# Kernel tuning notes

Hardware: AMD Instinct MI355X
Metric: run time of the kernel (lower is better)

## Reference

```python
import jax, jax.numpy as jnp
import numpy as np

B, S, E, H = 2, 1024, 1024, 16
Dh = E // H


def setup_inputs() -> dict:
    key = jax.random.key(0)
    ks = jax.random.split(key, 32)
    sc = 1.0 / np.sqrt(E)  # xavier-ish scale
    inp = {}
    names_x = ["x_q_a", "x_q_b", "x_kv_a", "x_kv_b"]
    for i, n in enumerate(names_x):
        inp[n] = jax.random.normal(ks[i], (B, S, E), jnp.float32)
    # causal mask, broadcastable to (B, H, S, S); masked where == 0
    inp["mask"] = jnp.tril(jnp.ones((S, S), jnp.int32))[None, None, :, :]
    inp["layer_theta"] = jnp.float32(0.3)
    inp["thetas_head"] = 0.1 * jax.random.normal(ks[4], (H,), jnp.float32)
    i = 5
    for p in ["q", "k", "v", "o"]:
        inp[p + "_wa"] = sc * jax.random.normal(ks[i], (E, E), jnp.float32); i += 1
        inp[p + "_wb"] = sc * jax.random.normal(ks[i], (E, E), jnp.float32); i += 1
        inp[p + "_ba"] = jnp.zeros((E,), jnp.float32)
        inp[p + "_bb"] = jnp.zeros((E,), jnp.float32)
    return inp


def _qc_dense(xa, xb, wa, wb, ba, bb, j2):
    # F.linear: x @ W.T + b ; j2 is a scalar so (Wb*j2) factors out
    out_a = xa @ wa.T + ba + (xb @ wb.T) * j2
    out_b = xa @ wb.T + bb + xb @ wa.T
    return out_a, out_b


def _shape(x):
    # (B,S,E) -> (B,H,S,Dh)
    return x.reshape(B, S, H, Dh).transpose(0, 2, 1, 3)


def _unshape(x):
    return x.transpose(0, 2, 1, 3).reshape(B, S, E)


def _rope(x):
    # standard rotate-half RoPE on last dim, positions over axis -2
    inv_freq = 1.0 / (10000.0 ** (jnp.arange(0, Dh, 2, dtype=jnp.float32) / Dh))
    ang = jnp.arange(S, dtype=jnp.float32)[:, None] * inv_freq[None, :]  # (S, Dh/2)
    cos = jnp.concatenate([jnp.cos(ang), jnp.cos(ang)], axis=-1)  # (S, Dh)
    sin = jnp.concatenate([jnp.sin(ang), jnp.sin(ang)], axis=-1)
    x1, x2 = x[..., : Dh // 2], x[..., Dh // 2:]
    rot = jnp.concatenate([-x2, x1], axis=-1)
    return x * cos + rot * sin


def reference(x_q_a, x_q_b, x_kv_a, x_kv_b, mask, layer_theta, thetas_head,
              q_wa, q_wb, q_ba, q_bb, k_wa, k_wb, k_ba, k_bb,
              v_wa, v_wb, v_ba, v_bb, o_wa, o_wb, o_ba, o_bb):
    j2 = jnp.sin(2.0 * layer_theta) - 1.0
    qa, qb = _qc_dense(x_q_a, x_q_b, q_wa, q_wb, q_ba, q_bb, j2)
    ka, kb = _qc_dense(x_kv_a, x_kv_b, k_wa, k_wb, k_ba, k_bb, j2)
    va, vb = _qc_dense(x_kv_a, x_kv_b, v_wa, v_wb, v_ba, v_bb, j2)
    qa, qb = _rope(_shape(qa)), _rope(_shape(qb))
    ka, kb = _rope(_shape(ka)), _rope(_shape(kb))
    va, vb = _shape(va), _shape(vb)
    j2h = (jnp.sin(2.0 * thetas_head) - 1.0).reshape(1, H, 1, 1)
    # dual QC score matrices (B,H,S,S)
    s_a = jnp.einsum("bhqd,bhkd->bhqk", qa, ka) + jnp.einsum("bhqd,bhkd->bhqk", qb, kb) * j2h
    s_b = jnp.einsum("bhqd,bhkd->bhqk", qa, kb) + jnp.einsum("bhqd,bhkd->bhqk", qb, ka)
    mag = jnp.sqrt(s_a * s_a + s_b * s_b + 1e-8) / np.sqrt(Dh)
    mag = jnp.where(mask == 0, -1e9, mag)
    attn = jax.nn.softmax(mag, axis=-1)
    out_a = _unshape(jnp.einsum("bhqk,bhkd->bhqd", attn, va))
    out_b = _unshape(jnp.einsum("bhqk,bhkd->bhqd", attn, vb))
    return _qc_dense(out_a, out_b, o_wa, o_wb, o_ba, o_bb, j2)
```

## Files before the change

kernel.cpp:

```cpp
#include <hip/hip_runtime.h>
#include <math.h>
#include <stdint.h>

#define BATCH 2
#define SEQ   1024
#define EMB   1024
#define NH    16
#define DH    64
#define BSE   (BATCH*SEQ*EMB)
#define MROWS (BATCH*SEQ)

typedef unsigned short u16;
typedef __attribute__((ext_vector_type(8))) short short8;
typedef __attribute__((ext_vector_type(4))) float f32x4;

__device__ __forceinline__ float bf2f(u16 u) {
    return __uint_as_float(((unsigned int)u) << 16);
}
__device__ __forceinline__ u16 f2bf(float f) {
    unsigned int x = __float_as_uint(f);
    x += 0x7FFFu + ((x >> 16) & 1u);
    return (u16)(x >> 16);
}

__device__ __forceinline__ void async_copy16(const void* g, void* l) {
    __builtin_amdgcn_global_load_lds(
        (const __attribute__((address_space(1))) unsigned int*)g,
        (__attribute__((address_space(3))) unsigned int*)l,
        16, 0, 0);
}

struct PackArgs {
    const float* src[20];
    u16*         dst[20];
    int          scaled[20];
};

__global__ __launch_bounds__(256) void pack_kernel(PackArgs pa, const float* __restrict__ theta)
{
    const int e = blockIdx.y;
    const size_t i = ((size_t)blockIdx.x * 256 + threadIdx.x) * 4;
    float sc = 1.0f;
    if (pa.scaled[e]) sc = sinf(2.0f * theta[0]) - 1.0f;
    float4 v = *(const float4*)(pa.src[e] + i);
    ushort4 o;
    o.x = f2bf(v.x * sc); o.y = f2bf(v.y * sc);
    o.z = f2bf(v.z * sc); o.w = f2bf(v.w * sc);
    *(ushort4*)(pa.dst[e] + i) = o;
}

struct GemmArgs {
    const u16*   A1s[8];
    const u16*   A2s[8];
    const u16*   Blo[8];
    const u16*   Bhi[8];
    const float* bias[8];
    void*        dst[8];
    int          mode[8];
};

template<int SPLITK>
__global__ __launch_bounds__(256) void mfma_gemm(GemmArgs ga)
{
    __shared__ u16 sA[128][32];
    __shared__ u16 sB[128][32];

    const int t    = threadIdx.x;
    const int lane = t & 63;
    const int w    = t >> 6;
    const int wx   = w & 1;
    const int wy   = w >> 1;
    const int n0   = blockIdx.y * 128;
    const int m0   = blockIdx.x * 128;
    const int ko   = (SPLITK == 2) ? blockIdx.z : 0;
    const int seg  = n0 >> 10;
    const int nloc = n0 & 1023;

    const int srow = t >> 2;
    const int sb   = (t & 3) * 16;

    f32x4 acc[4][4] = {};

    const char* A1 = (const char*)ga.A1s[seg];
    const char* A2 = (const char*)ga.A2s[seg];
    const char* Bl = (const char*)ga.Blo[seg];
    const char* Bh = (const char*)ga.Bhi[seg];
    if (SPLITK == 2 && ko) { A1 = A2; Bl = Bh; }

    const int frow = lane & 15;
    const int quad = lane >> 4;

    const int NKT = (SPLITK == 2) ? 32 : 64;
    for (int kt = 0; kt < NKT; ++kt) {
        const char* As = (SPLITK == 1 && (kt & 32)) ? A2 : A1;
        const char* Bs = (SPLITK == 1 && (kt & 32)) ? Bh : Bl;
        const size_t kbyte = (size_t)(kt & 31) * 64;

        __syncthreads();
        #pragma unroll
        for (int r = 0; r < 2; ++r) {
            const int row = r*64 + srow;
            const int ldsoff = (r*64 + w*16) * 64;
            async_copy16(As + (size_t)(m0 + row)*2048 + kbyte + sb,
                         (char*)&sA[0][0] + ldsoff);
            async_copy16(Bs + (size_t)(nloc + row)*2048 + kbyte + sb,
                         (char*)&sB[0][0] + ldsoff);
        }
        __syncthreads();

        short8 af[4], bfr[4];
        #pragma unroll
        for (int i = 0; i < 4; ++i)
            af[i] = *(const short8*)&sA[wy*64 + i*16 + frow][quad*8];
        #pragma unroll
        for (int j = 0; j < 4; ++j)
            bfr[j] = *(const short8*)&sB[wx*64 + j*16 + frow][quad*8];

        #pragma unroll
        for (int i = 0; i < 4; ++i)
            #pragma unroll
            for (int j = 0; j < 4; ++j)
                acc[i][j] = __builtin_amdgcn_mfma_f32_16x16x32_bf16(
                                af[i], bfr[j], acc[i][j], 0, 0, 0);
    }

    const float* bias = ga.bias[seg];
    const int mode = ga.mode[seg];

    #pragma unroll
    for (int j = 0; j < 4; ++j) {
        const int c = nloc + wx*64 + j*16 + frow;
        const float bv = (SPLITK == 2 && ko) ? 0.0f : bias[c];
        #pragma unroll
        for (int i = 0; i < 4; ++i) {
            #pragma unroll
            for (int reg = 0; reg < 4; ++reg) {
                const int m = m0 + wy*64 + i*16 + quad*4 + reg;
                const float val = acc[i][j][reg] + bv;
                if (mode == 1) {
                    if (SPLITK == 2)
                        atomicAdd((float*)ga.dst[seg] + (size_t)m*1024 + c, val);
                    else
                        ((float*)ga.dst[seg])[(size_t)m*1024 + c] = val;
                } else if (mode == 2) {
                    ((u16*)ga.dst[seg])[((size_t)(m >> 10) << 20) + (size_t)c*1024 + (m & 1023)] = f2bf(val);
                } else {
                    ((u16*)ga.dst[seg])[(size_t)m*1024 + c] = f2bf(val);
                }
            }
        }
    }
}

__global__ __launch_bounds__(256) void rope_kernel(
    u16* qa, u16* qb, u16* ka, u16* kb)
{
    u16* p;
    switch (blockIdx.y) {
        case 0:  p = qa; break;
        case 1:  p = qb; break;
        case 2:  p = ka; break;
        default: p = kb; break;
    }
    const int i   = blockIdx.x * 256 + threadIdx.x;
    const int d   = i & 31;
    const int hh  = (i >> 5) & (NH - 1);
    const int row = i >> 9;
    const int s   = row & (SEQ - 1);
    const size_t base = (size_t)row * EMB + hh * DH;

    float x1 = bf2f(p[base + d]);
    float x2 = bf2f(p[base + d + 32]);
    const float invf_rev = expf(-(float)d * 0.28782313662425576f) * 0.15915494309189535f;
    float rev = (float)s * invf_rev;
    rev -= floorf(rev);
    const float sn = __builtin_amdgcn_sinf(rev);
    const float cs = __builtin_amdgcn_cosf(rev);
    p[base + d]      = f2bf(x1 * cs - x2 * sn);
    p[base + d + 32] = f2bf(x2 * cs + x1 * sn);
}

__global__ __launch_bounds__(256) void attn_mfma(
    const u16* __restrict__ qa, const u16* __restrict__ qb,
    const u16* __restrict__ ka, const u16* __restrict__ kb,
    const u16* __restrict__ vat, const u16* __restrict__ vbt,
    const float* __restrict__ thetas,
    u16* __restrict__ oa, u16* __restrict__ ob)
{
    __shared__ u16 sKa[64][64];
    __shared__ u16 sKb[64][64];
    __shared__ u16 sVa[64][64];
    __shared__ u16 sVb[64][64];
    __shared__ u16 sP[4][16][72];

    const int t    = threadIdx.x;
    const int lane = t & 63;
    const int w    = t >> 6;
    const int L15  = lane & 15;
    const int quad = lane >> 4;

    const int bid  = blockIdx.x;
    const int aa   = (bid >> 5) & 7;
    const int qt   = (bid >> 8) ? aa : (15 - aa);
    const int bh   = bid & 31;
    const int h    = bh & 15;
    const int b    = bh >> 4;

    const float j2h = sinf(2.0f * thetas[h]) - 1.0f;

    const int   qrow  = qt*64 + w*16 + L15;
    const size_t qbase = (size_t)(b*SEQ + qrow) * EMB + h*DH;
    short8 fqa[2], fqb[2], fjqb[2];
    fqa[0] = *(const short8*)(qa + qbase + quad*8);
    fqa[1] = *(const short8*)(qa + qbase + 32 + quad*8);
    fqb[0] = *(const short8*)(qb + qbase + quad*8);
    fqb[1] = *(const short8*)(qb + qbase + 32 + quad*8);
    #pragma unroll
    for (int s2 = 0; s2 < 2; ++s2) {
        short8 src = fqb[s2], dst;
        #pragma unroll
        for (int j = 0; j < 8; ++j)
            dst[j] = (short)f2bf(bf2f((u16)src[j]) * j2h);
        fjqb[s2] = dst;
    }

    f32x4 acc_a[4] = {};
    f32x4 acc_b[4] = {};
    float l_lane[4] = {0.f, 0.f, 0.f, 0.f};

    const int subrow = lane >> 3;
    const int g      = (lane & 7) ^ subrow;
    const int swz    = L15 & 7;

    for (int kt = 0; kt <= qt; ++kt) {
        __syncthreads();
        #pragma unroll
        for (int i = 0; i < 2; ++i) {
            const int row = w*16 + i*8 + subrow;
            const int ldsoff = (w*16 + i*8) * 128;
            const size_t ktok = (size_t)(b*SEQ + kt*64 + row);
            async_copy16((const char*)ka + ktok*2048 + h*128 + g*16,
                         (char*)&sKa[0][0] + ldsoff);
            async_copy16((const char*)kb + ktok*2048 + h*128 + g*16,
                         (char*)&sKb[0][0] + ldsoff);
            const size_t vrow = (size_t)b*1048576 + (size_t)(h*64 + row)*1024 + kt*64;
            async_copy16((const char*)vat + vrow*2 + g*16,
                         (char*)&sVa[0][0] + ldsoff);
            async_copy16((const char*)vbt + vrow*2 + g*16,
                         (char*)&sVb[0][0] + ldsoff);
        }
        __syncthreads();

        f32x4 sa[4] = {}, sb[4] = {};
        #pragma unroll
        for (int n = 0; n < 4; ++n) {
            const u16* rKa = &sKa[n*16 + L15][0];
            const u16* rKb = &sKb[n*16 + L15][0];
            short8 ka0 = *(const short8*)(rKa + (( quad      ^ swz) << 3));
            short8 ka1 = *(const short8*)(rKa + (((4 + quad) ^ swz) << 3));
            short8 kb0 = *(const short8*)(rKb + (( quad      ^ swz) << 3));
            short8 kb1 = *(const short8*)(rKb + (((4 + quad) ^ swz) << 3));
            sa[n] = __builtin_amdgcn_mfma_f32_16x16x32_bf16(fqa[0],  ka0, sa[n], 0, 0, 0);
            sa[n] = __builtin_amdgcn_mfma_f32_16x16x32_bf16(fqa[1],  ka1, sa[n], 0, 0, 0);
            sa[n] = __builtin_amdgcn_mfma_f32_16x16x32_bf16(fjqb[0], kb0, sa[n], 0, 0, 0);
            sa[n] = __builtin_amdgcn_mfma_f32_16x16x32_bf16(fjqb[1], kb1, sa[n], 0, 0, 0);
            sb[n] = __builtin_amdgcn_mfma_f32_16x16x32_bf16(fqa[0],  kb0, sb[n], 0, 0, 0);
            sb[n] = __builtin_amdgcn_mfma_f32_16x16x32_bf16(fqa[1],  kb1, sb[n], 0, 0, 0);
            sb[n] = __builtin_amdgcn_mfma_f32_16x16x32_bf16(fqb[0],  ka0, sb[n], 0, 0, 0);
            sb[n] = __builtin_amdgcn_mfma_f32_16x16x32_bf16(fqb[1],  ka1, sb[n], 0, 0, 0);
        }

        float p[4][4];
        if (kt == qt) {
            #pragma unroll
            for (int n = 0; n < 4; ++n)
                #pragma unroll
                for (int r = 0; r < 4; ++r) {
                    const float A = sa[n][r], B = sb[n][r];
                    const float mag = __builtin_amdgcn_sqrtf(A*A + B*B + 1e-8f) * 0.125f;
                    const bool masked = (n*16 + L15) > (w*16 + quad*4 + r);
                    p[n][r] = masked ? 0.0f
                                     : __builtin_amdgcn_exp2f(mag * 1.44269504f);
                }
        } else {
            #pragma unroll
            for (int n = 0; n < 4; ++n)
                #pragma unroll
                for (int r = 0; r < 4; ++r) {
                    const float A = sa[n][r], B = sb[n][r];
                    const float mag = __builtin_amdgcn_sqrtf(A*A + B*B + 1e-8f) * 0.125f;
                    p[n][r] = __builtin_amdgcn_exp2f(mag * 1.44269504f);
                }
        }
        #pragma unroll
        for (int r = 0; r < 4; ++r)
            l_lane[r] += (p[0][r] + p[1][r]) + (p[2][r] + p[3][r]);

        #pragma unroll
        for (int n = 0; n < 4; ++n)
            #pragma unroll
            for (int r = 0; r < 4; ++r)
                sP[w][quad*4 + r][n*16 + L15] = f2bf(p[n][r]);

        short8 pf0 = *(const short8*)&sP[w][L15][quad*8];
        short8 pf1 = *(const short8*)&sP[w][L15][32 + quad*8];

        #pragma unroll
        for (int n = 0; n < 4; ++n) {
            const u16* rVa = &sVa[n*16 + L15][0];
            const u16* rVb = &sVb[n*16 + L15][0];
            short8 va0 = *(const short8*)(rVa + (( quad      ^ swz) << 3));
            short8 va1 = *(const short8*)(rVa + (((4 + quad) ^ swz) << 3));
            short8 vb0 = *(const short8*)(rVb + (( quad      ^ swz) << 3));
            short8 vb1 = *(const short8*)(rVb + (((4 + quad) ^ swz) << 3));
            acc_a[n] = __builtin_amdgcn_mfma_f32_16x16x32_bf16(pf0, va0, acc_a[n], 0, 0, 0);
            acc_a[n] = __builtin_amdgcn_mfma_f32_16x16x32_bf16(pf1, va1, acc_a[n], 0, 0, 0);
            acc_b[n] = __builtin_amdgcn_mfma_f32_16x16x32_bf16(pf0, vb0, acc_b[n], 0, 0, 0);
            acc_b[n] = __builtin_amdgcn_mfma_f32_16x16x32_bf16(pf1, vb1, acc_b[n], 0, 0, 0);
        }
    }

    float inv[4];
    #pragma unroll
    for (int r = 0; r < 4; ++r) {
        float l = l_lane[r];
        #pragma unroll
        for (int off = 8; off >= 1; off >>= 1)
            l += __shfl_xor(l, off, 64);
        inv[r] = 1.0f / l;
    }

    #pragma unroll
    for (int reg = 0; reg < 4; ++reg) {
        const size_t tok = (size_t)(b*SEQ + qt*64 + w*16 + quad*4 + reg);
        #pragma unroll
        for (int n = 0; n < 4; ++n) {
            const size_t idx = tok*EMB + h*DH + n*16 + L15;
            oa[idx] = f2bf(acc_a[n][reg] * inv[reg]);
            ob[idx] = f2bf(acc_b[n][reg] * inv[reg]);
        }
    }
}

extern "C" void kernel_launch(void* const* d_in, const int* in_sizes, int n_in,
                              void* d_out, int out_size, void* d_ws, size_t ws_size,
                              hipStream_t stream)
{
    const float* x_q_a  = (const float*)d_in[0];
    const float* x_q_b  = (const float*)d_in[1];
    const float* x_kv_a = (const float*)d_in[2];
    const float* x_kv_b = (const float*)d_in[3];
    const float* theta    = (const float*)d_in[5];
    const float* thetas_h = (const float*)d_in[6];
    const float* q_wa = (const float*)d_in[7];
    const float* q_wb = (const float*)d_in[8];
    const float* q_ba = (const float*)d_in[9];
    const float* q_bb = (const float*)d_in[10];
    const float* k_wa = (const float*)d_in[11];
    const float* k_wb = (const float*)d_in[12];
    const float* k_ba = (const float*)d_in[13];
    const float* k_bb = (const float*)d_in[14];
    const float* v_wa = (const float*)d_in[15];
    const float* v_wb = (const float*)d_in[16];
    const float* v_ba = (const float*)d_in[17];
    const float* v_bb = (const float*)d_in[18];
    const float* o_wa = (const float*)d_in[19];
    const float* o_wb = (const float*)d_in[20];
    const float* o_ba = (const float*)d_in[21];
    const float* o_bb = (const float*)d_in[22];

    u16* W = (u16*)d_ws;
    const size_t XN = (size_t)BSE;
    const size_t WN = (size_t)EMB*EMB;
    u16* xq_a16  = W;
    u16* xq_b16  = W + XN;
    u16* xkv_a16 = W + 2*XN;
    u16* xkv_b16 = W + 3*XN;
    u16* wbase   = W + 4*XN;
    u16* q_wa16  = wbase;
    u16* q_wb16  = wbase + WN;
    u16* k_wa16  = wbase + 2*WN;
    u16* k_wb16  = wbase + 3*WN;
    u16* v_wa16  = wbase + 4*WN;
    u16* v_wb16  = wbase + 5*WN;
    u16* o_wa16  = wbase + 6*WN;
    u16* o_wb16  = wbase + 7*WN;
    u16* q_wbs16 = wbase + 8*WN;
    u16* k_wbs16 = wbase + 9*WN;
    u16* v_wbs16 = wbase + 10*WN;
    u16* o_wbs16 = wbase + 11*WN;
    u16* qkv     = wbase + 12*WN;
    u16* qa16 = qkv;
    u16* qb16 = qkv + XN;
    u16* ka16 = qkv + 2*XN;
    u16* kb16 = qkv + 3*XN;
    u16* vat16 = qkv + 4*XN;
    u16* vbt16 = qkv + 5*XN;
    u16* ao16 = xq_a16;
    u16* bo16 = xq_b16;

    float* out_a = (float*)d_out;
    float* out_b = out_a + (size_t)BSE;

    PackArgs pa;
    int si = 0;
    auto add = [&](const float* s, u16* d, int scaled, int chunks) {
        for (int c = 0; c < chunks; ++c) {
            pa.src[si] = s + (size_t)c * WN;
            pa.dst[si] = d + (size_t)c * WN;
            pa.scaled[si] = scaled;
            ++si;
        }
    };
    add(x_q_a,  xq_a16,  0, 2);
    add(x_q_b,  xq_b16,  0, 2);
    add(x_kv_a, xkv_a16, 0, 2);
    add(x_kv_b, xkv_b16, 0, 2);
    add(q_wa, q_wa16, 0, 1);  add(q_wb, q_wb16, 0, 1);
    add(k_wa, k_wa16, 0, 1);  add(k_wb, k_wb16, 0, 1);
    add(v_wa, v_wa16, 0, 1);  add(v_wb, v_wb16, 0, 1);
    add(o_wa, o_wa16, 0, 1);  add(o_wb, o_wb16, 0, 1);
    add(q_wb, q_wbs16, 1, 1); add(k_wb, k_wbs16, 1, 1);
    add(v_wb, v_wbs16, 1, 1); add(o_wb, o_wbs16, 1, 1);
    pack_kernel<<<dim3(WN/1024, 20), 256, 0, stream>>>(pa, theta);

    hipMemsetAsync(d_out, 0, (size_t)out_size * sizeof(float), stream);

    GemmArgs g12;
    const u16* a1s[6] = { xq_a16, xq_a16, xkv_a16, xkv_a16, xkv_a16, xkv_a16 };
    const u16* a2s[6] = { xq_b16, xq_b16, xkv_b16, xkv_b16, xkv_b16, xkv_b16 };
    const u16* blo[6] = { q_wa16, q_wb16, k_wa16, k_wb16, v_wa16, v_wb16 };
    const u16* bhi[6] = { q_wbs16, q_wa16, k_wbs16, k_wa16, v_wbs16, v_wa16 };
    const float* bia[6] = { q_ba, q_bb, k_ba, k_bb, v_ba, v_bb };
    void* dsts[6] = { qa16, qb16, ka16, kb16, vat16, vbt16 };
    const int modes[6] = { 0, 0, 0, 0, 2, 2 };
    for (int s = 0; s < 6; ++s) {
        g12.A1s[s] = a1s[s]; g12.A2s[s] = a2s[s];
        g12.Blo[s] = blo[s]; g12.Bhi[s] = bhi[s];
        g12.bias[s] = bia[s]; g12.dst[s] = dsts[s]; g12.mode[s] = modes[s];
    }
    for (int s = 6; s < 8; ++s) {
        g12.A1s[s] = a1s[0]; g12.A2s[s] = a2s[0];
        g12.Blo[s] = blo[0]; g12.Bhi[s] = bhi[0];
        g12.bias[s] = bia[0]; g12.dst[s] = dsts[0]; g12.mode[s] = 0;
    }
    mfma_gemm<1><<<dim3(MROWS/128, 48), 256, 0, stream>>>(g12);

    rope_kernel<<<dim3((BATCH*SEQ*NH*32)/256, 4), 256, 0, stream>>>(qa16, qb16, ka16, kb16);

    attn_mfma<<<BATCH*NH*(SEQ/64), 256, 0, stream>>>(qa16, qb16, ka16, kb16,
                                                     vat16, vbt16, thetas_h, ao16, bo16);

    GemmArgs g3;
    for (int s = 0; s < 8; ++s) {
        g3.A1s[s] = ao16; g3.A2s[s] = bo16;
        g3.Blo[s] = o_wa16; g3.Bhi[s] = o_wbs16;
        g3.bias[s] = o_ba; g3.dst[s] = out_a; g3.mode[s] = 1;
    }
    g3.Blo[1] = o_wb16; g3.Bhi[1] = o_wa16; g3.bias[1] = o_bb; g3.dst[1] = out_b;
    mfma_gemm<2><<<dim3(MROWS/128, 16, 2), 256, 0, stream>>>(g3);
}
```

Measured before the change: 308.1 us.

## Fuse RoPE into attention kernel and fold output zeroing into pack kernel

Removes the standalone RoPE kernel. Rotary embedding is now applied in registers: to Q fragments when they are loaded, and to each K tile before it is written to swizzled, padded LDS. The memset of the output buffer is replaced by extra zero-fill slices in the pack kernel, which saves one launch. In exchange, K loads become synchronous register loads instead of async global-to-LDS copies, and sin/cos for K is recomputed for every query tile that visits it.

```diff
diff --git a/kernel.cpp b/kernel.cpp
--- a/kernel.cpp
+++ b/kernel.cpp
@@ -30,23 +30,32 @@
         16, 0, 0);
 }
 
+#define ROPE_L2   0.4152410118609203f
+#define INV2PI    0.15915494309189535f
+
 struct PackArgs {
-    const float* src[20];
-    u16*         dst[20];
-    int          scaled[20];
+    const float* src[24];
+    void*        dst[24];
+    int          scaled[24];
 };
 
 __global__ __launch_bounds__(256) void pack_kernel(PackArgs pa, const float* __restrict__ theta)
 {
     const int e = blockIdx.y;
     const size_t i = ((size_t)blockIdx.x * 256 + threadIdx.x) * 4;
+    const int sm = pa.scaled[e];
+    if (sm < 0) {
+        float4 z = {0.f, 0.f, 0.f, 0.f};
+        *(float4*)((float*)pa.dst[e] + i) = z;
+        return;
+    }
     float sc = 1.0f;
-    if (pa.scaled[e]) sc = sinf(2.0f * theta[0]) - 1.0f;
+    if (sm) sc = sinf(2.0f * theta[0]) - 1.0f;
     float4 v = *(const float4*)(pa.src[e] + i);
     ushort4 o;
     o.x = f2bf(v.x * sc); o.y = f2bf(v.y * sc);
     o.z = f2bf(v.z * sc); o.w = f2bf(v.w * sc);
-    *(ushort4*)(pa.dst[e] + i) = o;
+    *(ushort4*)((u16*)pa.dst[e] + i) = o;
 }
 
 struct GemmArgs {
@@ -152,34 +161,6 @@
     }
 }
 
-__global__ __launch_bounds__(256) void rope_kernel(
-    u16* qa, u16* qb, u16* ka, u16* kb)
-{
-    u16* p;
-    switch (blockIdx.y) {
-        case 0:  p = qa; break;
-        case 1:  p = qb; break;
-        case 2:  p = ka; break;
-        default: p = kb; break;
-    }
-    const int i   = blockIdx.x * 256 + threadIdx.x;
-    const int d   = i & 31;
-    const int hh  = (i >> 5) & (NH - 1);
-    const int row = i >> 9;
-    const int s   = row & (SEQ - 1);
-    const size_t base = (size_t)row * EMB + hh * DH;
-
-    float x1 = bf2f(p[base + d]);
-    float x2 = bf2f(p[base + d + 32]);
-    const float invf_rev = expf(-(float)d * 0.28782313662425576f) * 0.15915494309189535f;
-    float rev = (float)s * invf_rev;
-    rev -= floorf(rev);
-    const float sn = __builtin_amdgcn_sinf(rev);
-    const float cs = __builtin_amdgcn_cosf(rev);
-    p[base + d]      = f2bf(x1 * cs - x2 * sn);
-    p[base + d + 32] = f2bf(x2 * cs + x1 * sn);
-}
-
 __global__ __launch_bounds__(256) void attn_mfma(
     const u16* __restrict__ qa, const u16* __restrict__ qb,
     const u16* __restrict__ ka, const u16* __restrict__ kb,
@@ -187,8 +168,8 @@
     const float* __restrict__ thetas,
     u16* __restrict__ oa, u16* __restrict__ ob)
 {
-    __shared__ u16 sKa[64][64];
-    __shared__ u16 sKb[64][64];
+    __shared__ u16 sKa[64][72];
+    __shared__ u16 sKb[64][72];
     __shared__ u16 sVa[64][64];
     __shared__ u16 sVb[64][64];
     __shared__ u16 sP[4][16][72];
@@ -210,18 +191,26 @@
 
     const int   qrow  = qt*64 + w*16 + L15;
     const size_t qbase = (size_t)(b*SEQ + qrow) * EMB + h*DH;
+    short8 ra0 = *(const short8*)(qa + qbase + quad*8);
+    short8 ra1 = *(const short8*)(qa + qbase + 32 + quad*8);
+    short8 rb0 = *(const short8*)(qb + qbase + quad*8);
+    short8 rb1 = *(const short8*)(qb + qbase + 32 + quad*8);
     short8 fqa[2], fqb[2], fjqb[2];
-    fqa[0] = *(const short8*)(qa + qbase + quad*8);
-    fqa[1] = *(const short8*)(qa + qbase + 32 + quad*8);
-    fqb[0] = *(const short8*)(qb + qbase + quad*8);
-    fqb[1] = *(const short8*)(qb + qbase + 32 + quad*8);
     #pragma unroll
-    for (int s2 = 0; s2 < 2; ++s2) {
-        short8 src = fqb[s2], dst;
-        #pragma unroll
-        for (int j = 0; j < 8; ++j)
-            dst[j] = (short)f2bf(bf2f((u16)src[j]) * j2h);
-        fjqb[s2] = dst;
+    for (int j = 0; j < 8; ++j) {
+        const int d = quad*8 + j;
+        const float invf = __builtin_amdgcn_exp2f(-(float)d * ROPE_L2) * INV2PI;
+        float rev = (float)qrow * invf;
+        rev -= floorf(rev);
+        const float sn = __builtin_amdgcn_sinf(rev);
+        const float cs = __builtin_amdgcn_cosf(rev);
+        const float a1 = bf2f((u16)ra0[j]), a2 = bf2f((u16)ra1[j]);
+        const float b1 = bf2f((u16)rb0[j]), b2 = bf2f((u16)rb1[j]);
+        const float na1 = a1*cs - a2*sn, na2 = a2*cs + a1*sn;
+        const float nb1 = b1*cs - b2*sn, nb2 = b2*cs + b1*sn;
+        fqa[0][j]  = (short)f2bf(na1);       fqa[1][j]  = (short)f2bf(na2);
+        fqb[0][j]  = (short)f2bf(nb1);       fqb[1][j]  = (short)f2bf(nb2);
+        fjqb[0][j] = (short)f2bf(nb1 * j2h); fjqb[1][j] = (short)f2bf(nb2 * j2h);
     }
 
     f32x4 acc_a[4] = {};
@@ -232,22 +221,53 @@
     const int g      = (lane & 7) ^ subrow;
     const int swz    = L15 & 7;
 
+    const int krow  = t >> 2;
+    const int ku    = t & 3;
+    const int glow  = (ku ^ (krow & 7)) & 3;
+    const int sl_lo = glow ^ (krow & 7);
+    const int sl_hi = sl_lo ^ 4;
+    float kinvf[8];
+    #pragma unroll
+    for (int j = 0; j < 8; ++j)
+        kinvf[j] = __builtin_amdgcn_exp2f(-(float)(glow*8 + j) * ROPE_L2) * INV2PI;
+
     for (int kt = 0; kt <= qt; ++kt) {
         __syncthreads();
         #pragma unroll
         for (int i = 0; i < 2; ++i) {
             const int row = w*16 + i*8 + subrow;
             const int ldsoff = (w*16 + i*8) * 128;
-            const size_t ktok = (size_t)(b*SEQ + kt*64 + row);
-            async_copy16((const char*)ka + ktok*2048 + h*128 + g*16,
-                         (char*)&sKa[0][0] + ldsoff);
-            async_copy16((const char*)kb + ktok*2048 + h*128 + g*16,
-                         (char*)&sKb[0][0] + ldsoff);
             const size_t vrow = (size_t)b*1048576 + (size_t)(h*64 + row)*1024 + kt*64;
             async_copy16((const char*)vat + vrow*2 + g*16,
                          (char*)&sVa[0][0] + ldsoff);
             async_copy16((const char*)vbt + vrow*2 + g*16,
                          (char*)&sVb[0][0] + ldsoff);
+        }
+        {
+            const int   skey  = kt*64 + krow;
+            const size_t kadr = (size_t)(b*SEQ + skey) * EMB + h*DH + glow*8;
+            short8 alo = *(const short8*)(ka + kadr);
+            short8 ahi = *(const short8*)(ka + kadr + 32);
+            short8 blo = *(const short8*)(kb + kadr);
+            short8 bhi = *(const short8*)(kb + kadr + 32);
+            short8 walo, wahi, wblo, wbhi;
+            #pragma unroll
+            for (int j = 0; j < 8; ++j) {
+                float rev = (float)skey * kinvf[j];
+                rev -= floorf(rev);
+                const float sn = __builtin_amdgcn_sinf(rev);
+                const float cs = __builtin_amdgcn_cosf(rev);
+                const float a1 = bf2f((u16)alo[j]), a2 = bf2f((u16)ahi[j]);
+                const float b1 = bf2f((u16)blo[j]), b2 = bf2f((u16)bhi[j]);
+                walo[j] = (short)f2bf(a1*cs - a2*sn);
+                wahi[j] = (short)f2bf(a2*cs + a1*sn);
+                wblo[j] = (short)f2bf(b1*cs - b2*sn);
+                wbhi[j] = (short)f2bf(b2*cs + b1*sn);
+            }
+            *(short8*)&sKa[krow][sl_lo*8] = walo;
+            *(short8*)&sKa[krow][sl_hi*8] = wahi;
+            *(short8*)&sKb[krow][sl_lo*8] = wblo;
+            *(short8*)&sKb[krow][sl_hi*8] = wbhi;
         }
         __syncthreads();
 
@@ -404,10 +424,11 @@
 
     PackArgs pa;
     int si = 0;
-    auto add = [&](const float* s, u16* d, int scaled, int chunks) {
+    auto add = [&](const void* s, void* d, int scaled, int chunks) {
         for (int c = 0; c < chunks; ++c) {
-            pa.src[si] = s + (size_t)c * WN;
-            pa.dst[si] = d + (size_t)c * WN;
+            pa.src[si] = (const float*)s + (size_t)c * WN;
+            pa.dst[si] = (scaled < 0) ? (void*)((float*)d + (size_t)c * WN)
+                                      : (void*)((u16*)d + (size_t)c * WN);
             pa.scaled[si] = scaled;
             ++si;
         }
@@ -422,9 +443,8 @@
     add(o_wa, o_wa16, 0, 1);  add(o_wb, o_wb16, 0, 1);
     add(q_wb, q_wbs16, 1, 1); add(k_wb, k_wbs16, 1, 1);
     add(v_wb, v_wbs16, 1, 1); add(o_wb, o_wbs16, 1, 1);
-    pack_kernel<<<dim3(WN/1024, 20), 256, 0, stream>>>(pa, theta);
-
-    hipMemsetAsync(d_out, 0, (size_t)out_size * sizeof(float), stream);
+    add(nullptr, d_out, -1, 4);
+    pack_kernel<<<dim3(WN/1024, 24), 256, 0, stream>>>(pa, theta);
 
     GemmArgs g12;
     const u16* a1s[6] = { xq_a16, xq_a16, xkv_a16, xkv_a16, xkv_a16, xkv_a16 };
@@ -446,8 +466,6 @@
     }
     mfma_gemm<1><<<dim3(MROWS/128, 48), 256, 0, stream>>>(g12);
 
-    rope_kernel<<<dim3((BATCH*SEQ*NH*32)/256, 4), 256, 0, stream>>>(qa16, qb16, ka16, kb16);
-
     attn_mfma<<<BATCH*NH*(SEQ/64), 256, 0, stream>>>(qa16, qb16, ka16, kb16,
                                                      vat16, vbt16, thetas_h, ao16, bo16);
 
```

Result: no change. 308.6 us (+0.2%).

## Fuse RoPE into QKV GEMM epilogue, fold memset into pack, split-K 4

Applied to the files above, without the earlier changes.

Applies rotary embedding directly on the GEMM accumulators for Q/K segments, removing the separate RoPE kernel and its bf16 read/write pass. The output zero-fill moves into the pack kernel instead of a separate memset. The QKV GEMM grid is remapped so consecutive blocks share an M tile for L2 reuse. The output projection uses split-K of 4 for more parallelism, at the cost of more atomic adds.

```diff
diff --git a/kernel.cpp b/kernel.cpp
--- a/kernel.cpp
+++ b/kernel.cpp
@@ -30,23 +30,32 @@
         16, 0, 0);
 }
 
+#define ROPE_L2   0.4152410118609203f
+#define INV2PI    0.15915494309189535f
+
 struct PackArgs {
-    const float* src[20];
-    u16*         dst[20];
-    int          scaled[20];
+    const float* src[24];
+    void*        dst[24];
+    int          scaled[24];
 };
 
 __global__ __launch_bounds__(256) void pack_kernel(PackArgs pa, const float* __restrict__ theta)
 {
     const int e = blockIdx.y;
     const size_t i = ((size_t)blockIdx.x * 256 + threadIdx.x) * 4;
+    const int sm = pa.scaled[e];
+    if (sm < 0) {
+        float4 z = {0.f, 0.f, 0.f, 0.f};
+        *(float4*)((float*)pa.dst[e] + i) = z;
+        return;
+    }
     float sc = 1.0f;
-    if (pa.scaled[e]) sc = sinf(2.0f * theta[0]) - 1.0f;
+    if (sm) sc = sinf(2.0f * theta[0]) - 1.0f;
     float4 v = *(const float4*)(pa.src[e] + i);
     ushort4 o;
     o.x = f2bf(v.x * sc); o.y = f2bf(v.y * sc);
     o.z = f2bf(v.z * sc); o.w = f2bf(v.w * sc);
-    *(ushort4*)(pa.dst[e] + i) = o;
+    *(ushort4*)((u16*)pa.dst[e] + i) = o;
 }
 
 struct GemmArgs {
@@ -70,9 +79,19 @@
     const int w    = t >> 6;
     const int wx   = w & 1;
     const int wy   = w >> 1;
-    const int n0   = blockIdx.y * 128;
-    const int m0   = blockIdx.x * 128;
-    const int ko   = (SPLITK == 2) ? blockIdx.z : 0;
+
+    int bx, by;
+    if (SPLITK == 1) {
+        const int id = blockIdx.x + (blockIdx.y << 4);
+        bx = id / 48;
+        by = id % 48;
+    } else {
+        bx = blockIdx.x;
+        by = blockIdx.y;
+    }
+    const int n0   = by * 128;
+    const int m0   = bx * 128;
+    const int ko   = (SPLITK > 1) ? blockIdx.z : 0;
     const int seg  = n0 >> 10;
     const int nloc = n0 & 1023;
 
@@ -85,16 +104,20 @@
     const char* A2 = (const char*)ga.A2s[seg];
     const char* Bl = (const char*)ga.Blo[seg];
     const char* Bh = (const char*)ga.Bhi[seg];
-    if (SPLITK == 2 && ko) { A1 = A2; Bl = Bh; }
+    size_t kbase = 0;
+    if (SPLITK == 4) {
+        if (ko >= 2) { A1 = A2; Bl = Bh; }
+        kbase = (size_t)(ko & 1) * 1024;
+    }
 
     const int frow = lane & 15;
     const int quad = lane >> 4;
 
-    const int NKT = (SPLITK == 2) ? 32 : 64;
+    const int NKT = 64 / SPLITK;
     for (int kt = 0; kt < NKT; ++kt) {
         const char* As = (SPLITK == 1 && (kt & 32)) ? A2 : A1;
         const char* Bs = (SPLITK == 1 && (kt & 32)) ? Bh : Bl;
-        const size_t kbyte = (size_t)(kt & 31) * 64;
+        const size_t kbyte = kbase + (size_t)(kt & 31) * 64;
 
         __syncthreads();
         #pragma unroll
@@ -130,15 +153,48 @@
     #pragma unroll
     for (int j = 0; j < 4; ++j) {
         const int c = nloc + wx*64 + j*16 + frow;
-        const float bv = (SPLITK == 2 && ko) ? 0.0f : bias[c];
+        const float bv = (SPLITK > 1 && ko) ? 0.0f : bias[c];
+        #pragma unroll
+        for (int i = 0; i < 4; ++i)
+            #pragma unroll
+            for (int reg = 0; reg < 4; ++reg)
+                acc[i][j][reg] += bv;
+    }
+
+    if (mode == 3) {
+        #pragma unroll
+        for (int jj = 0; jj < 2; ++jj) {
+            const float invf_rev = __builtin_amdgcn_exp2f(
+                                       -(float)(jj*16 + frow) * ROPE_L2) * INV2PI;
+            #pragma unroll
+            for (int i = 0; i < 4; ++i) {
+                #pragma unroll
+                for (int reg = 0; reg < 4; ++reg) {
+                    const int m = m0 + wy*64 + i*16 + quad*4 + reg;
+                    float rev = (float)(m & (SEQ-1)) * invf_rev;
+                    rev -= floorf(rev);
+                    const float sn = __builtin_amdgcn_sinf(rev);
+                    const float cs = __builtin_amdgcn_cosf(rev);
+                    const float x1 = acc[i][jj][reg];
+                    const float x2 = acc[i][jj+2][reg];
+                    acc[i][jj][reg]   = x1*cs - x2*sn;
+                    acc[i][jj+2][reg] = x2*cs + x1*sn;
+                }
+            }
+        }
+    }
+
+    #pragma unroll
+    for (int j = 0; j < 4; ++j) {
+        const int c = nloc + wx*64 + j*16 + frow;
         #pragma unroll
         for (int i = 0; i < 4; ++i) {
             #pragma unroll
             for (int reg = 0; reg < 4; ++reg) {
                 const int m = m0 + wy*64 + i*16 + quad*4 + reg;
-                const float val = acc[i][j][reg] + bv;
+                const float val = acc[i][j][reg];
                 if (mode == 1) {
-                    if (SPLITK == 2)
+                    if (SPLITK > 1)
                         atomicAdd((float*)ga.dst[seg] + (size_t)m*1024 + c, val);
                     else
                         ((float*)ga.dst[seg])[(size_t)m*1024 + c] = val;
@@ -150,34 +206,6 @@
             }
         }
     }
-}
-
-__global__ __launch_bounds__(256) void rope_kernel(
-    u16* qa, u16* qb, u16* ka, u16* kb)
-{
-    u16* p;
-    switch (blockIdx.y) {
-        case 0:  p = qa; break;
-        case 1:  p = qb; break;
-        case 2:  p = ka; break;
-        default: p = kb; break;
-    }
-    const int i   = blockIdx.x * 256 + threadIdx.x;
-    const int d   = i & 31;
-    const int hh  = (i >> 5) & (NH - 1);
-    const int row = i >> 9;
-    const int s   = row & (SEQ - 1);
-    const size_t base = (size_t)row * EMB + hh * DH;
-
-    float x1 = bf2f(p[base + d]);
-    float x2 = bf2f(p[base + d + 32]);
-    const float invf_rev = expf(-(float)d * 0.28782313662425576f) * 0.15915494309189535f;
-    float rev = (float)s * invf_rev;
-    rev -= floorf(rev);
-    const float sn = __builtin_amdgcn_sinf(rev);
-    const float cs = __builtin_amdgcn_cosf(rev);
-    p[base + d]      = f2bf(x1 * cs - x2 * sn);
-    p[base + d + 32] = f2bf(x2 * cs + x1 * sn);
 }
 
 __global__ __launch_bounds__(256) void attn_mfma(
@@ -404,10 +432,11 @@
 
     PackArgs pa;
     int si = 0;
-    auto add = [&](const float* s, u16* d, int scaled, int chunks) {
+    auto add = [&](const void* s, void* d, int scaled, int chunks) {
         for (int c = 0; c < chunks; ++c) {
-            pa.src[si] = s + (size_t)c * WN;
-            pa.dst[si] = d + (size_t)c * WN;
+            pa.src[si] = (const float*)s + (size_t)c * WN;
+            pa.dst[si] = (scaled < 0) ? (void*)((float*)d + (size_t)c * WN)
+                                      : (void*)((u16*)d + (size_t)c * WN);
             pa.scaled[si] = scaled;
             ++si;
         }
@@ -422,9 +451,8 @@
     add(o_wa, o_wa16, 0, 1);  add(o_wb, o_wb16, 0, 1);
     add(q_wb, q_wbs16, 1, 1); add(k_wb, k_wbs16, 1, 1);
     add(v_wb, v_wbs16, 1, 1); add(o_wb, o_wbs16, 1, 1);
-    pack_kernel<<<dim3(WN/1024, 20), 256, 0, stream>>>(pa, theta);
-
-    hipMemsetAsync(d_out, 0, (size_t)out_size * sizeof(float), stream);
+    add(nullptr, d_out, -1, 4);
+    pack_kernel<<<dim3(WN/1024, 24), 256, 0, stream>>>(pa, theta);
 
     GemmArgs g12;
     const u16* a1s[6] = { xq_a16, xq_a16, xkv_a16, xkv_a16, xkv_a16, xkv_a16 };
@@ -433,7 +461,7 @@
     const u16* bhi[6] = { q_wbs16, q_wa16, k_wbs16, k_wa16, v_wbs16, v_wa16 };
     const float* bia[6] = { q_ba, q_bb, k_ba, k_bb, v_ba, v_bb };
     void* dsts[6] = { qa16, qb16, ka16, kb16, vat16, vbt16 };
-    const int modes[6] = { 0, 0, 0, 0, 2, 2 };
+    const int modes[6] = { 3, 3, 3, 3, 2, 2 };
     for (int s = 0; s < 6; ++s) {
         g12.A1s[s] = a1s[s]; g12.A2s[s] = a2s[s];
         g12.Blo[s] = blo[s]; g12.Bhi[s] = bhi[s];
@@ -445,8 +473,6 @@
         g12.bias[s] = bia[0]; g12.dst[s] = dsts[0]; g12.mode[s] = 0;
     }
     mfma_gemm<1><<<dim3(MROWS/128, 48), 256, 0, stream>>>(g12);
-
-    rope_kernel<<<dim3((BATCH*SEQ*NH*32)/256, 4), 256, 0, stream>>>(qa16, qb16, ka16, kb16);
 
     attn_mfma<<<BATCH*NH*(SEQ/64), 256, 0, stream>>>(qa16, qb16, ka16, kb16,
                                                      vat16, vbt16, thetas_h, ao16, bo16);
@@ -458,5 +484,5 @@
         g3.bias[s] = o_ba; g3.dst[s] = out_a; g3.mode[s] = 1;
     }
     g3.Blo[1] = o_wb16; g3.Bhi[1] = o_wa16; g3.bias[1] = o_bb; g3.dst[1] = out_b;
-    mfma_gemm<2><<<dim3(MROWS/128, 16, 2), 256, 0, stream>>>(g3);
-}
+    mfma_gemm<4><<<dim3(MROWS/128, 16, 4), 256, 0, stream>>>(g3);
+}
```

After: 355.8 us. 1.15x slower.
